# Kernel optimization log

Measured on AMD Instinct MI355X. Metric: run time of the kernel, lower is better.

## Reference

```python
import jax, jax.numpy as jnp
import numpy as np

N_EMBD = 1024
N_HEAD = 16
HEAD_DIM = N_EMBD // N_HEAD
B, T = 4, 2048


def setup_inputs() -> dict:
    key = jax.random.key(0)
    ks = jax.random.split(key, 5)
    s_in = 1.0 / np.sqrt(N_EMBD)
    return {
        "x": jax.random.normal(ks[0], (B, T, N_EMBD), dtype=jnp.float32),
        "w_attn": jax.random.normal(ks[1], (N_EMBD, 3 * N_EMBD), dtype=jnp.float32) * s_in,
        "b_attn": jnp.zeros((3 * N_EMBD,), dtype=jnp.float32),
        "w_proj": jax.random.normal(ks[2], (N_EMBD, N_EMBD), dtype=jnp.float32) * s_in,
        "b_proj": jnp.zeros((N_EMBD,), dtype=jnp.float32),
    }


def reference(x, w_attn, b_attn, w_proj, b_proj):
    b, t, c = x.shape
    qkv = x @ w_attn + b_attn                      # [B,T,3C]
    q, k, v = jnp.split(qkv, 3, axis=-1)
    # [B,T,C] -> [B,H,T,D]
    def heads(z):
        return z.reshape(b, t, N_HEAD, HEAD_DIM).transpose(0, 2, 1, 3)
    q, k, v = heads(q), heads(k), heads(v)
    scale = 1.0 / np.sqrt(HEAD_DIM)
    att = jnp.einsum("bhqd,bhkd->bhqk", q, k) * scale
    causal = jnp.tril(jnp.ones((t, t), dtype=bool))
    att = jnp.where(causal, att, -jnp.inf)
    att = jax.nn.softmax(att, axis=-1)
    y = jnp.einsum("bhqk,bhkd->bhqd", att, v)      # [B,H,T,D]
    y = y.transpose(0, 2, 1, 3).reshape(b, t, c)
    return y @ w_proj + b_proj
```

## Files before the change

### kernel.cpp

```cpp
#include <hip/hip_runtime.h>
#include <hip/hip_bf16.h>

#define B_  4
#define T_  2048
#define C_  1024
#define H_  16
#define D_  64
#define C3_ 3072

typedef __attribute__((ext_vector_type(8))) short bf16x8;
typedef __attribute__((ext_vector_type(4))) float f32x4;
typedef unsigned short u16;

#define CSCALE 0.1803368801111204f

__device__ __forceinline__ u16 f2bf(float f) {
  union { float f; unsigned int u; } v; v.f = f;
  unsigned int r = (v.u + 0x7FFFu + ((v.u >> 16) & 1u)) >> 16;
  return (u16)r;
}

__device__ __forceinline__ void gload16(void* l, const void* g) {
  __builtin_amdgcn_global_load_lds(
      (const __attribute__((address_space(1))) unsigned int*)g,
      (__attribute__((address_space(3))) unsigned int*)l, 16, 0, 0);
}

__global__ __launch_bounds__(256)
void cvt_bf16(const float* __restrict__ in, u16* __restrict__ out, int n8) {
  int i = blockIdx.x * 256 + threadIdx.x;
  if (i >= n8) return;
  float4 a = *(const float4*)(in + (size_t)i * 8);
  float4 b = *(const float4*)(in + (size_t)i * 8 + 4);
  ushort4 lo, hi;
  lo.x = f2bf(a.x); lo.y = f2bf(a.y); lo.z = f2bf(a.z); lo.w = f2bf(a.w);
  hi.x = f2bf(b.x); hi.y = f2bf(b.y); hi.z = f2bf(b.z); hi.w = f2bf(b.w);
  *(ushort4*)(out + (size_t)i * 8) = lo;
  *(ushort4*)(out + (size_t)i * 8 + 4) = hi;
}

__global__ __launch_bounds__(256)
void transcvt(const float* __restrict__ w, u16* __restrict__ wT, int K, int N) {
  int n  = blockIdx.x * 64 + (threadIdx.x & 63);
  int k0 = blockIdx.y * 16 + (threadIdx.x >> 6) * 4;
  float v0 = w[(size_t)(k0 + 0) * N + n];
  float v1 = w[(size_t)(k0 + 1) * N + n];
  float v2 = w[(size_t)(k0 + 2) * N + n];
  float v3 = w[(size_t)(k0 + 3) * N + n];
  ushort4 o; o.x = f2bf(v0); o.y = f2bf(v1); o.z = f2bf(v2); o.w = f2bf(v3);
  *(ushort4*)(wT + (size_t)n * K + k0) = o;
}

__global__ __launch_bounds__(256)
void vtrans(const u16* __restrict__ qkv, u16* __restrict__ vT) {
  const int bid = blockIdx.x;
  const int bh = bid >> 6, tc = bid & 63;
  const int d = threadIdx.x & 63, t4 = threadIdx.x >> 6;
  const int t8 = tc * 4 + t4;
  const int b = bh >> 4, h = bh & 15;
  const u16* src = qkv + (size_t)(b * T_ + t8 * 8) * C3_ + 2 * C_ + h * 64 + d;
  union { u16 a[8]; int4 v; } u;
#pragma unroll
  for (int e = 0; e < 8; ++e) u.a[e] = src[(size_t)e * C3_];
  *(int4*)(vT + ((size_t)bh * 64 + d) * T_ + t8 * 8) = u.v;
}

template <typename OutT>
__global__ __launch_bounds__(512, 2)
void gemm256(const u16* __restrict__ A, const u16* __restrict__ Bt,
             const float* __restrict__ bias, OutT* __restrict__ C,
             int M, int N, int K, int qscale_cols) {
  __shared__ int4 lds[8192];

  const int tid = threadIdx.x, lane = tid & 63, wid = tid >> 6;
  const int wr = wid >> 2, wc = wid & 3;
  const int row0 = blockIdx.y * 256, col0 = blockIdx.x * 256;

  f32x4 acc[8][4];
#pragma unroll
  for (int m = 0; m < 8; ++m)
#pragma unroll
    for (int nf = 0; nf < 4; ++nf) acc[m][nf] = (f32x4){0.f, 0.f, 0.f, 0.f};

  const u16* pA[2][2]; const u16* pB[2][2];
#pragma unroll
  for (int h = 0; h < 2; ++h)
#pragma unroll
    for (int i = 0; i < 2; ++i) {
      int g = h * 1024 + i * 512 + tid;
      int rr = ((g >> 7) << 4) + (g & 15), ko = ((g >> 4) & 7) * 8;
      pA[h][i] = A + (size_t)(row0 + rr) * K + ko;
      pB[h][i] = Bt + (size_t)(col0 + rr) * K + ko;
    }

  auto stage = [&](int t, int isA, int h, int buf) {
    const u16* p0 = (isA ? pA[h][0] : pB[h][0]) + t * 64;
    const u16* p1 = (isA ? pA[h][1] : pB[h][1]) + t * 64;
    int4* d = &lds[buf * 4096 + (isA ? 0 : 2048) + h * 1024 + wid * 64];
    gload16(d, p0);
    gload16(d + 512, p1);
  };
  auto rdA = [&](int f, int kk, int buf) {
    return *(const bf16x8*)&lds[buf * 4096 + (wr * 8 + f) * 128 + kk * 64 + lane];
  };
  auto rdB = [&](int nf, int kk, int buf) {
    return *(const bf16x8*)&lds[buf * 4096 + 2048 + (wc * 4 + nf) * 128 + kk * 64 + lane];
  };

  const int nk = K >> 6, nit = nk >> 1;

  stage(0, 1, 0, 0); stage(0, 1, 1, 0); stage(0, 0, 0, 0); stage(0, 0, 1, 0);
  stage(1, 0, 0, 1); stage(1, 0, 1, 1); stage(1, 1, 0, 1);
  asm volatile("s_waitcnt vmcnt(6)" ::: "memory");
  __builtin_amdgcn_s_barrier();

  for (int it = 0; it < nit; ++it) {
    const int t1g = 2 * it + 1, t2g = t1g + 1, t3g = t1g + 2;
    bf16x8 a0[4][2], a1[4][2], b0[2][2], b1[2][2];

#pragma unroll
    for (int m = 0; m < 4; ++m) { a0[m][0] = rdA(m, 0, 0); a0[m][1] = rdA(m, 1, 0); }
#pragma unroll
    for (int nf = 0; nf < 2; ++nf) { b0[nf][0] = rdB(nf, 0, 0); b0[nf][1] = rdB(nf, 1, 0); }
    stage(t1g, 1, 1, 1);
    __builtin_amdgcn_s_barrier();
    __builtin_amdgcn_s_setprio(1);
#pragma unroll
    for (int m = 0; m < 4; ++m)
#pragma unroll
      for (int nf = 0; nf < 2; ++nf) {
        acc[m][nf] = __builtin_amdgcn_mfma_f32_16x16x32_bf16(a0[m][0], b0[nf][0], acc[m][nf], 0, 0, 0);
        acc[m][nf] = __builtin_amdgcn_mfma_f32_16x16x32_bf16(a0[m][1], b0[nf][1], acc[m][nf], 0, 0, 0);
      }
    __builtin_amdgcn_s_setprio(0);
    __builtin_amdgcn_s_barrier();

#pragma unroll
    for (int nf = 0; nf < 2; ++nf) { b1[nf][0] = rdB(2 + nf, 0, 0); b1[nf][1] = rdB(2 + nf, 1, 0); }
    __builtin_amdgcn_s_barrier();
    __builtin_amdgcn_s_setprio(1);
#pragma unroll
    for (int m = 0; m < 4; ++m)
#pragma unroll
      for (int nf = 0; nf < 2; ++nf) {
        acc[m][2 + nf] = __builtin_amdgcn_mfma_f32_16x16x32_bf16(a0[m][0], b1[nf][0], acc[m][2 + nf], 0, 0, 0);
        acc[m][2 + nf] = __builtin_amdgcn_mfma_f32_16x16x32_bf16(a0[m][1], b1[nf][1], acc[m][2 + nf], 0, 0, 0);
      }
    __builtin_amdgcn_s_setprio(0);
    __builtin_amdgcn_s_barrier();

#pragma unroll
    for (int m = 0; m < 4; ++m) { a1[m][0] = rdA(4 + m, 0, 0); a1[m][1] = rdA(4 + m, 1, 0); }
    if (t2g < nk) stage(t2g, 0, 0, 0);
    __builtin_amdgcn_s_barrier();
    __builtin_amdgcn_s_setprio(1);
#pragma unroll
    for (int m = 0; m < 4; ++m)
#pragma unroll
      for (int nf = 0; nf < 2; ++nf) {
        acc[4 + m][2 + nf] = __builtin_amdgcn_mfma_f32_16x16x32_bf16(a1[m][0], b1[nf][0], acc[4 + m][2 + nf], 0, 0, 0);
        acc[4 + m][2 + nf] = __builtin_amdgcn_mfma_f32_16x16x32_bf16(a1[m][1], b1[nf][1], acc[4 + m][2 + nf], 0, 0, 0);
      }
    __builtin_amdgcn_s_setprio(0);
    __builtin_amdgcn_s_barrier();

    if (t2g < nk) {
      stage(t2g, 0, 1, 0);
      stage(t2g, 1, 0, 0);
      asm volatile("s_waitcnt vmcnt(6)" ::: "memory");
    } else {
      asm volatile("s_waitcnt vmcnt(0)" ::: "memory");
    }
    __builtin_amdgcn_s_barrier();
    __builtin_amdgcn_s_setprio(1);
#pragma unroll
    for (int m = 0; m < 4; ++m)
#pragma unroll
      for (int nf = 0; nf < 2; ++nf) {
        acc[4 + m][nf] = __builtin_amdgcn_mfma_f32_16x16x32_bf16(a1[m][0], b0[nf][0], acc[4 + m][nf], 0, 0, 0);
        acc[4 + m][nf] = __builtin_amdgcn_mfma_f32_16x16x32_bf16(a1[m][1], b0[nf][1], acc[4 + m][nf], 0, 0, 0);
      }
    __builtin_amdgcn_s_setprio(0);
    __builtin_amdgcn_s_barrier();

#pragma unroll
    for (int m = 0; m < 4; ++m) { a0[m][0] = rdA(m, 0, 1); a0[m][1] = rdA(m, 1, 1); }
#pragma unroll
    for (int nf = 0; nf < 2; ++nf) { b0[nf][0] = rdB(nf, 0, 1); b0[nf][1] = rdB(nf, 1, 1); }
    if (t2g < nk) stage(t2g, 1, 1, 0);
    __builtin_amdgcn_s_barrier();
    __builtin_amdgcn_s_setprio(1);
#pragma unroll
    for (int m = 0; m < 4; ++m)
#pragma unroll
      for (int nf = 0; nf < 2; ++nf) {
        acc[m][nf] = __builtin_amdgcn_mfma_f32_16x16x32_bf16(a0[m][0], b0[nf][0], acc[m][nf], 0, 0, 0);
        acc[m][nf] = __builtin_amdgcn_mfma_f32_16x16x32_bf16(a0[m][1], b0[nf][1], acc[m][nf], 0, 0, 0);
      }
    __builtin_amdgcn_s_setprio(0);
    __builtin_amdgcn_s_barrier();

#pragma unroll
    for (int nf = 0; nf < 2; ++nf) { b1[nf][0] = rdB(2 + nf, 0, 1); b1[nf][1] = rdB(2 + nf, 1, 1); }
    __builtin_amdgcn_s_barrier();
    __builtin_amdgcn_s_setprio(1);
#pragma unroll
    for (int m = 0; m < 4; ++m)
#pragma unroll
      for (int nf = 0; nf < 2; ++nf) {
        acc[m][2 + nf] = __builtin_amdgcn_mfma_f32_16x16x32_bf16(a0[m][0], b1[nf][0], acc[m][2 + nf], 0, 0, 0);
        acc[m][2 + nf] = __builtin_amdgcn_mfma_f32_16x16x32_bf16(a0[m][1], b1[nf][1], acc[m][2 + nf], 0, 0, 0);
      }
    __builtin_amdgcn_s_setprio(0);
    __builtin_amdgcn_s_barrier();

#pragma unroll
    for (int m = 0; m < 4; ++m) { a1[m][0] = rdA(4 + m, 0, 1); a1[m][1] = rdA(4 + m, 1, 1); }
    if (t3g < nk) stage(t3g, 0, 0, 1);
    __builtin_amdgcn_s_barrier();
    __builtin_amdgcn_s_setprio(1);
#pragma unroll
    for (int m = 0; m < 4; ++m)
#pragma unroll
      for (int nf = 0; nf < 2; ++nf) {
        acc[4 + m][2 + nf] = __builtin_amdgcn_mfma_f32_16x16x32_bf16(a1[m][0], b1[nf][0], acc[4 + m][2 + nf], 0, 0, 0);
        acc[4 + m][2 + nf] = __builtin_amdgcn_mfma_f32_16x16x32_bf16(a1[m][1], b1[nf][1], acc[4 + m][2 + nf], 0, 0, 0);
      }
    __builtin_amdgcn_s_setprio(0);
    __builtin_amdgcn_s_barrier();

    if (t3g < nk) {
      stage(t3g, 0, 1, 1);
      stage(t3g, 1, 0, 1);
      asm volatile("s_waitcnt vmcnt(6)" ::: "memory");
    } else {
      asm volatile("s_waitcnt vmcnt(0)" ::: "memory");
    }
    __builtin_amdgcn_s_barrier();
    __builtin_amdgcn_s_setprio(1);
#pragma unroll
    for (int m = 0; m < 4; ++m)
#pragma unroll
      for (int nf = 0; nf < 2; ++nf) {
        acc[4 + m][nf] = __builtin_amdgcn_mfma_f32_16x16x32_bf16(a1[m][0], b0[nf][0], acc[4 + m][nf], 0, 0, 0);
        acc[4 + m][nf] = __builtin_amdgcn_mfma_f32_16x16x32_bf16(a1[m][1], b0[nf][1], acc[4 + m][nf], 0, 0, 0);
      }
    __builtin_amdgcn_s_setprio(0);
    __builtin_amdgcn_s_barrier();
  }

  const int cc = lane & 15, qg = lane >> 4;
#pragma unroll
  for (int m = 0; m < 8; ++m) {
#pragma unroll
    for (int nf = 0; nf < 4; ++nf) {
      const int gc = col0 + wc * 64 + nf * 16 + cc;
      const float bv = bias[gc];
      const float sc = (gc < qscale_cols) ? CSCALE : 1.0f;
#pragma unroll
      for (int r = 0; r < 4; ++r) {
        const int gr = row0 + wr * 128 + m * 16 + qg * 4 + r;
        float val = (acc[m][nf][r] + bv) * sc;
        if constexpr (sizeof(OutT) == 2)
          ((u16*)C)[(size_t)gr * N + gc] = f2bf(val);
        else
          ((float*)C)[(size_t)gr * N + gc] = val;
      }
    }
  }
}

__global__ __launch_bounds__(512, 4)
void attn_mfma(const u16* __restrict__ qkv, const u16* __restrict__ vT,
               u16* __restrict__ yout) {
  __shared__ int4 Ks4[512];
  __shared__ int4 Vs4[512];
  __shared__ int4 Ps4[2048];

  const int n   = blockIdx.x;
  const int xcd = n & 7, t = n >> 3;
  const int bh  = xcd * 8 + (t >> 3);
  const int ip  = t & 7;
  const int b   = bh >> 4, h = bh & 15;

  const int tid = threadIdx.x;
  const int lane = tid & 63, wq = tid >> 6;
  const int sub = wq & 3;
  const int cc = lane & 15, qg = lane >> 4;

  const int qt128 = (wq < 4) ? ip : (15 - ip);
  const int qrow0 = qt128 * 128 + sub * 32;
  const int diag  = qt128 * 2 + (sub >> 1);
  const int jn    = 32 - 2 * ip;

  const u16* kbase = qkv + (size_t)b * T_ * C3_ + C_ + h * D_;
  const u16* vtb   = vT + (size_t)bh * D_ * T_;

  bf16x8 qf[2][2];
#pragma unroll
  for (int hf = 0; hf < 2; ++hf) {
    const u16* qb = qkv + (size_t)(b * T_ + qrow0 + hf * 16 + cc) * C3_ + h * D_;
    qf[hf][0] = *(const bf16x8*)(qb + qg * 8);
    qf[hf][1] = *(const bf16x8*)(qb + 32 + qg * 8);
  }

  const u16* kg = kbase + (size_t)((tid >> 7) * 16 + (tid & 15)) * C3_ +
                  ((tid >> 6) & 1) * 32 + ((tid >> 4) & 3) * 8;
  const u16* vg = vtb + (size_t)((tid >> 7) * 16 + (tid & 15)) * T_ +
                  ((tid >> 6) & 1) * 32 + ((tid >> 4) & 3) * 8;

  int4 kpref = *(const int4*)kg;
  int4 vpref = *(const int4*)vg;

  float m_r[2] = {-1e30f, -1e30f}, l_r[2] = {0.f, 0.f};
  f32x4 o[2][4];
#pragma unroll
  for (int hf = 0; hf < 2; ++hf)
#pragma unroll
    for (int db = 0; db < 4; ++db) o[hf][db] = (f32x4){0.f, 0.f, 0.f, 0.f};

  for (int j = 0; j < jn; ++j) {
    __syncthreads();
    Ks4[tid] = kpref;
    Vs4[tid] = vpref;
    __syncthreads();
    if (j + 1 < jn) {
      kpref = *(const int4*)(kg + (size_t)(j + 1) * 64 * C3_);
      vpref = *(const int4*)(vg + (j + 1) * 64);
    }
    if (j > diag) continue;

    __builtin_amdgcn_s_setprio(1);
    f32x4 s[2][4];
#pragma unroll
    for (int kb = 0; kb < 4; ++kb) {
      bf16x8 kf0 = *(const bf16x8*)(Ks4 + kb * 128 + lane);
      bf16x8 kf1 = *(const bf16x8*)(Ks4 + kb * 128 + 64 + lane);
#pragma unroll
      for (int hf = 0; hf < 2; ++hf) {
        f32x4 z = (f32x4){0.f, 0.f, 0.f, 0.f};
        z = __builtin_amdgcn_mfma_f32_16x16x32_bf16(kf0, qf[hf][0], z, 0, 0, 0);
        z = __builtin_amdgcn_mfma_f32_16x16x32_bf16(kf1, qf[hf][1], z, 0, 0, 0);
        s[hf][kb] = z;
      }
    }
    __builtin_amdgcn_s_setprio(0);

    if (j == diag) {
#pragma unroll
      for (int hf = 0; hf < 2; ++hf) {
        const int qabs = qrow0 + hf * 16 + cc;
#pragma unroll
        for (int kb = 0; kb < 4; ++kb)
#pragma unroll
          for (int r = 0; r < 4; ++r)
            if ((j * 64 + kb * 16 + qg * 4 + r) > qabs) s[hf][kb][r] = -1e30f;
      }
    }

#pragma unroll
    for (int hf = 0; hf < 2; ++hf) {
      float mx = s[hf][0][0];
#pragma unroll
      for (int kb = 0; kb < 4; ++kb)
#pragma unroll
        for (int r = 0; r < 4; ++r) mx = fmaxf(mx, s[hf][kb][r]);
      mx = fmaxf(mx, __shfl_xor(mx, 16));
      mx = fmaxf(mx, __shfl_xor(mx, 32));

      if (!__all(mx <= m_r[hf])) {
        float mn = fmaxf(m_r[hf], mx);
        float al = exp2f(m_r[hf] - mn);
        m_r[hf] = mn;
        l_r[hf] *= al;
        float alq[4];
#pragma unroll
        for (int r = 0; r < 4; ++r)
          alq[r] = __shfl(al, (lane & 48) | (qg * 4 + r));
#pragma unroll
        for (int db = 0; db < 4; ++db)
#pragma unroll
          for (int r = 0; r < 4; ++r) o[hf][db][r] *= alq[r];
      }

      float lsum = 0.f;
#pragma unroll
      for (int kb = 0; kb < 4; ++kb)
#pragma unroll
        for (int r = 0; r < 4; ++r) {
          float p = exp2f(s[hf][kb][r] - m_r[hf]);
          s[hf][kb][r] = p;
          lsum += p;
        }
      l_r[hf] += lsum;

      char* myPb = (char*)(Ps4 + wq * 256 + hf * 128);
#pragma unroll
      for (int kb = 0; kb < 4; ++kb) {
        unsigned plo, phi;
        asm("v_cvt_pk_bf16_f32 %0, %1, %2" : "=v"(plo) : "v"(s[hf][kb][0]), "v"(s[hf][kb][1]));
        asm("v_cvt_pk_bf16_f32 %0, %1, %2" : "=v"(phi) : "v"(s[hf][kb][2]), "v"(s[hf][kb][3]));
        const int kv0 = kb * 16 + qg * 4;
        const int g = ((kv0 >> 5) << 6) + (((kv0 >> 3) & 3) << 4) + cc;
        uint2 pk; pk.x = plo; pk.y = phi;
        *(uint2*)(myPb + g * 16 + (kv0 & 7) * 2) = pk;
      }
    }

    bf16x8 pa[2][2];
#pragma unroll
    for (int hf = 0; hf < 2; ++hf)
#pragma unroll
      for (int ks = 0; ks < 2; ++ks)
        pa[hf][ks] = *(const bf16x8*)(Ps4 + wq * 256 + hf * 128 + ks * 64 + lane);
    __builtin_amdgcn_s_setprio(1);
#pragma unroll
    for (int db = 0; db < 4; ++db) {
#pragma unroll
      for (int ks = 0; ks < 2; ++ks) {
        bf16x8 vf = *(const bf16x8*)(Vs4 + db * 128 + ks * 64 + lane);
        o[0][db] = __builtin_amdgcn_mfma_f32_16x16x32_bf16(pa[0][ks], vf, o[0][db], 0, 0, 0);
        o[1][db] = __builtin_amdgcn_mfma_f32_16x16x32_bf16(pa[1][ks], vf, o[1][db], 0, 0, 0);
      }
    }
    __builtin_amdgcn_s_setprio(0);
  }

#pragma unroll
  for (int hf = 0; hf < 2; ++hf) {
    float ls = l_r[hf];
    ls += __shfl_xor(ls, 16);
    ls += __shfl_xor(ls, 32);
    float linv_l = 1.0f / ls;
    float linv[4];
#pragma unroll
    for (int r = 0; r < 4; ++r)
      linv[r] = __shfl(linv_l, (lane & 48) | (qg * 4 + r));

    u16* yb = yout + (size_t)(b * T_ + qrow0 + hf * 16 + qg * 4) * C_ + h * D_ + cc;
#pragma unroll
    for (int db = 0; db < 4; ++db)
#pragma unroll
      for (int r = 0; r < 4; ++r)
        yb[(size_t)r * C_ + db * 16] = f2bf(o[hf][db][r] * linv[r]);
  }
}

extern "C" void kernel_launch(void* const* d_in, const int* in_sizes, int n_in,
                              void* d_out, int out_size, void* d_ws, size_t ws_size,
                              hipStream_t stream) {
  const float* x      = (const float*)d_in[0];
  const float* w_attn = (const float*)d_in[1];
  const float* b_attn = (const float*)d_in[2];
  const float* w_proj = (const float*)d_in[3];
  const float* b_proj = (const float*)d_in[4];
  float* out = (float*)d_out;

  char* ws = (char*)d_ws;
  u16* xb  = (u16*)(ws);
  u16* waT = (u16*)(ws + 16777216);
  u16* wpT = (u16*)(ws + 23068672);
  u16* qkv = (u16*)(ws + 25165824);
  u16* yb  = (u16*)(ws + 75497472);
  u16* vT  = (u16*)(ws + 92274688);

  cvt_bf16<<<4096, 256, 0, stream>>>(x, xb, (B_ * T_ * C_) / 8);
  transcvt<<<dim3(C3_ / 64, C_ / 16), 256, 0, stream>>>(w_attn, waT, C_, C3_);
  transcvt<<<dim3(C_ / 64, C_ / 16), 256, 0, stream>>>(w_proj, wpT, C_, C_);

  gemm256<u16><<<dim3(C3_ / 256, (B_ * T_) / 256), 512, 0, stream>>>(
      xb, waT, b_attn, qkv, B_ * T_, C3_, C_, C_);

  vtrans<<<4096, 256, 0, stream>>>(qkv, vT);

  attn_mfma<<<dim3(8 * H_ * B_), 512, 0, stream>>>(qkv, vT, yb);

  gemm256<float><<<dim3(C_ / 256, (B_ * T_) / 256), 512, 0, stream>>>(
      yb, wpT, b_proj, out, B_ * T_, C_, C_, 0);
}
```

Measured before the change: 224.3 us.

## Load K/V fragments directly from global memory and drop shared-memory staging

The attention kernel stops staging K and V tiles through shared memory with block-wide barriers and software prefetch. Each wave now reads its K and V MFMA fragments straight from global memory, relying on cache reuse. Blocks shrink to 256 threads each covering one 128-row query tile, launched longest-first, replacing the paired-tile load balancing. This removes the two barriers per iteration and the idle waves past the diagonal, at the cost of redundant global/L2 traffic and no explicit prefetch overlap.

```diff
diff --git a/kernel.cpp b/kernel.cpp
--- a/kernel.cpp
+++ b/kernel.cpp
@@ -270,28 +270,24 @@
   }
 }
 
-__global__ __launch_bounds__(512, 4)
+__global__ __launch_bounds__(256, 4)
 void attn_mfma(const u16* __restrict__ qkv, const u16* __restrict__ vT,
                u16* __restrict__ yout) {
-  __shared__ int4 Ks4[512];
-  __shared__ int4 Vs4[512];
-  __shared__ int4 Ps4[2048];
+  __shared__ int4 Ps4[4 * 256];
 
   const int n   = blockIdx.x;
   const int xcd = n & 7, t = n >> 3;
-  const int bh  = xcd * 8 + (t >> 3);
-  const int ip  = t & 7;
+  const int bhl = t >> 4;
+  const int qt  = 15 - (t & 15);
+  const int bh  = xcd * 8 + bhl;
   const int b   = bh >> 4, h = bh & 15;
 
   const int tid = threadIdx.x;
   const int lane = tid & 63, wq = tid >> 6;
-  const int sub = wq & 3;
   const int cc = lane & 15, qg = lane >> 4;
 
-  const int qt128 = (wq < 4) ? ip : (15 - ip);
-  const int qrow0 = qt128 * 128 + sub * 32;
-  const int diag  = qt128 * 2 + (sub >> 1);
-  const int jn    = 32 - 2 * ip;
+  const int qrow0 = qt * 128 + wq * 32;
+  const int diag  = qrow0 >> 6;
 
   const u16* kbase = qkv + (size_t)b * T_ * C3_ + C_ + h * D_;
   const u16* vtb   = vT + (size_t)bh * D_ * T_;
@@ -304,14 +300,6 @@
     qf[hf][1] = *(const bf16x8*)(qb + 32 + qg * 8);
   }
 
-  const u16* kg = kbase + (size_t)((tid >> 7) * 16 + (tid & 15)) * C3_ +
-                  ((tid >> 6) & 1) * 32 + ((tid >> 4) & 3) * 8;
-  const u16* vg = vtb + (size_t)((tid >> 7) * 16 + (tid & 15)) * T_ +
-                  ((tid >> 6) & 1) * 32 + ((tid >> 4) & 3) * 8;
-
-  int4 kpref = *(const int4*)kg;
-  int4 vpref = *(const int4*)vg;
-
   float m_r[2] = {-1e30f, -1e30f}, l_r[2] = {0.f, 0.f};
   f32x4 o[2][4];
 #pragma unroll
@@ -319,23 +307,15 @@
 #pragma unroll
     for (int db = 0; db < 4; ++db) o[hf][db] = (f32x4){0.f, 0.f, 0.f, 0.f};
 
-  for (int j = 0; j < jn; ++j) {
-    __syncthreads();
-    Ks4[tid] = kpref;
-    Vs4[tid] = vpref;
-    __syncthreads();
-    if (j + 1 < jn) {
-      kpref = *(const int4*)(kg + (size_t)(j + 1) * 64 * C3_);
-      vpref = *(const int4*)(vg + (j + 1) * 64);
-    }
-    if (j > diag) continue;
-
-    __builtin_amdgcn_s_setprio(1);
+  for (int j = 0; j <= diag; ++j) {
+    const u16* krow = kbase + (size_t)(j * 64 + cc) * C3_;
+    const u16* vrow = vtb + (size_t)cc * T_ + j * 64;
+
     f32x4 s[2][4];
 #pragma unroll
     for (int kb = 0; kb < 4; ++kb) {
-      bf16x8 kf0 = *(const bf16x8*)(Ks4 + kb * 128 + lane);
-      bf16x8 kf1 = *(const bf16x8*)(Ks4 + kb * 128 + 64 + lane);
+      bf16x8 kf0 = *(const bf16x8*)(krow + (size_t)kb * 16 * C3_ + qg * 8);
+      bf16x8 kf1 = *(const bf16x8*)(krow + (size_t)kb * 16 * C3_ + 32 + qg * 8);
 #pragma unroll
       for (int hf = 0; hf < 2; ++hf) {
         f32x4 z = (f32x4){0.f, 0.f, 0.f, 0.f};
@@ -344,7 +324,6 @@
         s[hf][kb] = z;
       }
     }
-    __builtin_amdgcn_s_setprio(0);
 
     if (j == diag) {
 #pragma unroll
@@ -413,17 +392,15 @@
 #pragma unroll
       for (int ks = 0; ks < 2; ++ks)
         pa[hf][ks] = *(const bf16x8*)(Ps4 + wq * 256 + hf * 128 + ks * 64 + lane);
-    __builtin_amdgcn_s_setprio(1);
 #pragma unroll
     for (int db = 0; db < 4; ++db) {
 #pragma unroll
       for (int ks = 0; ks < 2; ++ks) {
-        bf16x8 vf = *(const bf16x8*)(Vs4 + db * 128 + ks * 64 + lane);
+        bf16x8 vf = *(const bf16x8*)(vrow + (size_t)db * 16 * T_ + ks * 32 + qg * 8);
         o[0][db] = __builtin_amdgcn_mfma_f32_16x16x32_bf16(pa[0][ks], vf, o[0][db], 0, 0, 0);
         o[1][db] = __builtin_amdgcn_mfma_f32_16x16x32_bf16(pa[1][ks], vf, o[1][db], 0, 0, 0);
       }
     }
-    __builtin_amdgcn_s_setprio(0);
   }
 
 #pragma unroll
@@ -473,7 +450,7 @@
 
   vtrans<<<4096, 256, 0, stream>>>(qkv, vT);
 
-  attn_mfma<<<dim3(8 * H_ * B_), 512, 0, stream>>>(qkv, vT, yb);
+  attn_mfma<<<dim3(16 * H_ * B_), 256, 0, stream>>>(qkv, vT, yb);
 
   gemm256<float><<<dim3(C_ / 256, (B_ * T_) / 256), 512, 0, stream>>>(
       yb, wpT, b_proj, out, B_ * T_, C_, C_, 0);
```

Result: slower. 370.2 us (+65.0%).
